# Optimization experiments

Hardware: AMD Instinct MI355X
Metric: run time of the kernel (lower is better)

The kernel has to match this reference:

```python
import jax, jax.numpy as jnp
import numpy as np

DIM = 256
WIN = 64
HEADS = 8
HEAD_DIM = DIM // HEADS
SCALE = HEAD_DIM ** -0.5


def setup_inputs() -> dict:
    key = jax.random.key(0)
    ks = jax.random.split(key, 8)
    B_ = 4096
    nW = 64
    x = jax.random.normal(ks[0], (B_, WIN, DIM), dtype=jnp.float32)
    mask = jax.random.normal(ks[1], (nW, WIN, WIN), dtype=jnp.float32)
    # qkv Linear(dim, 3*dim): stored as [dim, 3*dim] for x @ w
    w_qkv = jax.random.normal(ks[2], (DIM, 3 * DIM), dtype=jnp.float32) * (DIM ** -0.5)
    b_qkv = jax.random.normal(ks[3], (3 * DIM,), dtype=jnp.float32) * 0.02
    w_proj = jax.random.normal(ks[4], (DIM, DIM), dtype=jnp.float32) * (DIM ** -0.5)
    b_proj = jax.random.normal(ks[5], (DIM,), dtype=jnp.float32) * 0.02
    # relative_position_bias_table: [2*window_size - 1, num_heads], trunc_normal std=0.02
    bias_table = jax.random.normal(ks[6], (2 * WIN - 1, HEADS), dtype=jnp.float32) * 0.02
    return {"x": x, "mask": mask, "w_qkv": w_qkv, "b_qkv": b_qkv,
            "w_proj": w_proj, "b_proj": b_proj, "bias_table": bias_table}


def reference(x, mask, w_qkv, b_qkv, w_proj, b_proj, bias_table):
    B_, N, C = x.shape
    # qkv projection -> [3, B_, H, N, hd]
    qkv = (x @ w_qkv + b_qkv).reshape(B_, N, 3, HEADS, HEAD_DIM)
    qkv = jnp.transpose(qkv, (2, 0, 3, 1, 4))
    q, k, v = qkv[0], qkv[1], qkv[2]
    attn = jnp.einsum('bhnd,bhmd->bhnm', q * SCALE, k)  # [B_, H, N, N]
    # relative position bias gather: index [N, N] into table [2N-1, H]
    coords = jnp.arange(N)
    rel_idx = coords[:, None] - coords[None, :] + (N - 1)  # [N, N]
    rel_bias = bias_table[rel_idx]  # [N, N, H]
    attn = attn + jnp.transpose(rel_bias, (2, 0, 1))[None]  # broadcast over B_
    # mask add: [nW, N, N] broadcast over batch groups and heads
    nW = mask.shape[0]
    attn = attn.reshape(B_ // nW, nW, HEADS, N, N) + mask[None, :, None]
    attn = attn.reshape(B_, HEADS, N, N)
    attn = jax.nn.softmax(attn, axis=-1)  # dropout is identity in eval
    out = jnp.einsum('bhnm,bhmd->bhnd', attn, v)
    out = jnp.transpose(out, (0, 2, 1, 3)).reshape(B_, N, C)
    return out @ w_proj + b_proj
```

## Files before the change

kernel.cpp:

```cpp
#include <hip/hip_runtime.h>
#include <hip/hip_bf16.h>

#define DIM 256
#define WIN 64
#define HEADS 8
#define HD 32
#define NW 64

typedef __attribute__((ext_vector_type(8))) short bf16x8;
typedef __attribute__((ext_vector_type(4))) float f32x4;

#define XS 264
#define QS 40
#define VS 72
#define PS 72
#define HREG 7424
#define LDS_ELEMS (WIN * XS + HEADS * HREG)

__device__ __forceinline__ unsigned short f2bf(float f) {
  union { float f; unsigned u; } v; v.f = f;
  unsigned r = v.u + 0x7FFFu + ((v.u >> 16) & 1u);
  return (unsigned short)(r >> 16);
}

__device__ __forceinline__ bf16x8 ldf(const unsigned short* p) {
  return *reinterpret_cast<const bf16x8*>(p);
}

#define MFMA16(a, b, c) __builtin_amdgcn_mfma_f32_16x16x32_bf16(a, b, c, 0, 0, 0)

__global__ void prep_kernel(const float* __restrict__ w_qkv,
                            const float* __restrict__ b_qkv,
                            const float* __restrict__ w_proj,
                            const float* __restrict__ bias_table,
                            unsigned short* __restrict__ wqkv_t,
                            unsigned short* __restrict__ wproj_t,
                            float* __restrict__ bqkv_s,
                            float* __restrict__ rb) {
  const float SCALE = 0.1767766952966369f;
  int idx = blockIdx.x * blockDim.x + threadIdx.x;
  if (idx < 768 * 256) {
    int n = idx >> 8, k = idx & 255;
    float v = w_qkv[k * 768 + n];
    if (n < 256) v *= SCALE;
    wqkv_t[idx] = f2bf(v);
  }
  if (idx < 256 * 256) {
    int n = idx >> 8, k = idx & 255;
    wproj_t[idx] = f2bf(w_proj[k * 256 + n]);
  }
  if (idx < 768) {
    float v = b_qkv[idx];
    if (idx < 256) v *= SCALE;
    bqkv_s[idx] = v;
  }
  if (idx < HEADS * WIN * WIN) {
    int h = idx >> 12;
    int r = idx & 4095;
    int n = r >> 6, m = r & 63;
    rb[idx] = bias_table[(n - m + WIN - 1) * HEADS + h];
  }
}

__global__ __launch_bounds__(1024, 4) void fused_attn(
    const float* __restrict__ x,
    const float* __restrict__ mask,
    const float* __restrict__ b_proj,
    const unsigned short* __restrict__ wqkv_t,
    const unsigned short* __restrict__ wproj_t,
    const float* __restrict__ bqkv_s,
    const float* __restrict__ rb,
    float* __restrict__ out) {
  extern __shared__ unsigned short lds[];
  unsigned short* xs = lds;
  const int tid = threadIdx.x;
  const int wave = tid >> 6;
  const int lane = tid & 63;
  const int l16 = lane & 15;
  const int quad = lane >> 4;
  const int b = blockIdx.x;
  const int h = wave >> 1;
  const int sub = wave & 1;

  unsigned short* qh = lds + WIN * XS + h * HREG;
  unsigned short* kh = qh + 64 * QS;
  unsigned short* vth = qh + 2 * 64 * QS;
  unsigned short* ph = qh;

  const float4* xg = reinterpret_cast<const float4*>(x + (size_t)b * (WIN * DIM));
#pragma unroll
  for (int i = 0; i < 4; ++i) {
    int e = tid + i * 1024;
    float4 f = xg[e];
    int n = e >> 6;
    int c = (e & 63) << 2;
    ushort4 s4;
    s4.x = f2bf(f.x); s4.y = f2bf(f.y); s4.z = f2bf(f.z); s4.w = f2bf(f.w);
    *reinterpret_cast<ushort4*>(xs + n * XS + c) = s4;
  }
  __syncthreads();

  {
    f32x4 acc[3][4];
#pragma unroll
    for (int c = 0; c < 3; ++c)
#pragma unroll
      for (int rt = 0; rt < 4; ++rt) acc[c][rt] = (f32x4){0.f, 0.f, 0.f, 0.f};

#pragma unroll
    for (int kk = 0; kk < 8; ++kk) {
      int k0 = kk * 32 + quad * 8;
      bf16x8 a[4], bb[3];
#pragma unroll
      for (int rt = 0; rt < 4; ++rt) a[rt] = ldf(xs + (rt * 16 + l16) * XS + k0);
#pragma unroll
      for (int c = 0; c < 3; ++c) {
        int ctp = sub * 3 + c;
        int cbase = h * 32 + (ctp >> 1) * 256 + (ctp & 1) * 16;
        bb[c] = ldf(wqkv_t + (cbase + l16) * 256 + k0);
      }
#pragma unroll
      for (int c = 0; c < 3; ++c)
#pragma unroll
        for (int rt = 0; rt < 4; ++rt) acc[c][rt] = MFMA16(a[rt], bb[c], acc[c][rt]);
    }

#pragma unroll
    for (int c = 0; c < 3; ++c) {
      int ctp = sub * 3 + c;
      int cbase = h * 32 + (ctp >> 1) * 256 + (ctp & 1) * 16;
      float bias = bqkv_s[cbase + l16];
#pragma unroll
      for (int rt = 0; rt < 4; ++rt)
#pragma unroll
        for (int r = 0; r < 4; ++r) {
          int row = rt * 16 + quad * 4 + r;
          unsigned short bv = f2bf(acc[c][rt][r] + bias);
          if (ctp < 2)      qh[row * QS + ctp * 16 + l16] = bv;
          else if (ctp < 4) kh[row * QS + (ctp - 2) * 16 + l16] = bv;
          else              vth[((ctp - 4) * 16 + l16) * VS + row] = bv;
        }
    }
  }
  __syncthreads();

  {
    f32x4 sacc[2][4];
#pragma unroll
    for (int rt = 0; rt < 2; ++rt)
#pragma unroll
      for (int ct = 0; ct < 4; ++ct) sacc[rt][ct] = (f32x4){0.f, 0.f, 0.f, 0.f};

    bf16x8 a[2], bb[4];
#pragma unroll
    for (int rt = 0; rt < 2; ++rt)
      a[rt] = ldf(qh + (sub * 32 + rt * 16 + l16) * QS + quad * 8);
#pragma unroll
    for (int ct = 0; ct < 4; ++ct) bb[ct] = ldf(kh + (ct * 16 + l16) * QS + quad * 8);
#pragma unroll
    for (int rt = 0; rt < 2; ++rt)
#pragma unroll
      for (int ct = 0; ct < 4; ++ct) sacc[rt][ct] = MFMA16(a[rt], bb[ct], sacc[rt][ct]);

    const float* rbh = rb + h * (WIN * WIN);
    const float* mw = mask + (size_t)(b & (NW - 1)) * (WIN * WIN);
#pragma unroll
    for (int rt = 0; rt < 2; ++rt) {
#pragma unroll
      for (int r = 0; r < 4; ++r) {
        int row = sub * 32 + rt * 16 + quad * 4 + r;
        float vals[4];
#pragma unroll
        for (int ct = 0; ct < 4; ++ct) {
          int col = ct * 16 + l16;
          vals[ct] = sacc[rt][ct][r] + rbh[row * 64 + col] + mw[row * 64 + col];
        }
        float m = fmaxf(fmaxf(vals[0], vals[1]), fmaxf(vals[2], vals[3]));
#pragma unroll
        for (int o = 1; o < 16; o <<= 1) m = fmaxf(m, __shfl_xor(m, o, 64));
        float s = 0.f;
#pragma unroll
        for (int ct = 0; ct < 4; ++ct) { vals[ct] = __expf(vals[ct] - m); s += vals[ct]; }
#pragma unroll
        for (int o = 1; o < 16; o <<= 1) s += __shfl_xor(s, o, 64);
        float inv = 1.0f / s;
#pragma unroll
        for (int ct = 0; ct < 4; ++ct)
          ph[row * PS + ct * 16 + l16] = f2bf(vals[ct] * inv);
      }
    }
  }

  {
    f32x4 oacc[2][2];
#pragma unroll
    for (int jt = 0; jt < 2; ++jt)
#pragma unroll
      for (int rt = 0; rt < 2; ++rt) oacc[jt][rt] = (f32x4){0.f, 0.f, 0.f, 0.f};

#pragma unroll
    for (int km = 0; km < 2; ++km) {
      int k0 = km * 32 + quad * 8;
      bf16x8 a[2], bb[2];
#pragma unroll
      for (int rt = 0; rt < 2; ++rt)
        a[rt] = ldf(ph + (sub * 32 + rt * 16 + l16) * PS + k0);
#pragma unroll
      for (int jt = 0; jt < 2; ++jt) bb[jt] = ldf(vth + (jt * 16 + l16) * VS + k0);
#pragma unroll
      for (int jt = 0; jt < 2; ++jt)
#pragma unroll
        for (int rt = 0; rt < 2; ++rt) oacc[jt][rt] = MFMA16(a[rt], bb[jt], oacc[jt][rt]);
    }
#pragma unroll
    for (int jt = 0; jt < 2; ++jt)
#pragma unroll
      for (int rt = 0; rt < 2; ++rt)
#pragma unroll
        for (int r = 0; r < 4; ++r) {
          int row = sub * 32 + rt * 16 + quad * 4 + r;
          xs[row * XS + h * 32 + jt * 16 + l16] = f2bf(oacc[jt][rt][r]);
        }
  }
  __syncthreads();

  {
    f32x4 pacc[4];
#pragma unroll
    for (int rt = 0; rt < 4; ++rt) pacc[rt] = (f32x4){0.f, 0.f, 0.f, 0.f};
    const int col = h * 32 + sub * 16 + l16;

#pragma unroll
    for (int kk = 0; kk < 8; ++kk) {
      int k0 = kk * 32 + quad * 8;
      bf16x8 a[4], bb;
#pragma unroll
      for (int rt = 0; rt < 4; ++rt) a[rt] = ldf(xs + (rt * 16 + l16) * XS + k0);
      bb = ldf(wproj_t + col * 256 + k0);
#pragma unroll
      for (int rt = 0; rt < 4; ++rt) pacc[rt] = MFMA16(a[rt], bb, pacc[rt]);
    }
    float bias = b_proj[col];
#pragma unroll
    for (int rt = 0; rt < 4; ++rt)
#pragma unroll
      for (int r = 0; r < 4; ++r) {
        int row = rt * 16 + quad * 4 + r;
        out[(size_t)(b * WIN + row) * DIM + col] = pacc[rt][r] + bias;
      }
  }
}

extern "C" void kernel_launch(void* const* d_in, const int* in_sizes, int n_in,
                              void* d_out, int out_size, void* d_ws, size_t ws_size,
                              hipStream_t stream) {
  const float* x          = (const float*)d_in[0];
  const float* mask       = (const float*)d_in[1];
  const float* w_qkv      = (const float*)d_in[2];
  const float* b_qkv      = (const float*)d_in[3];
  const float* w_proj     = (const float*)d_in[4];
  const float* b_proj     = (const float*)d_in[5];
  const float* bias_table = (const float*)d_in[6];

  unsigned short* wqkv_t  = (unsigned short*)d_ws;
  unsigned short* wproj_t = wqkv_t + 768 * 256;
  float* bqkv_s           = (float*)(wproj_t + 256 * 256);
  float* rb               = bqkv_s + 768;

  prep_kernel<<<768, 256, 0, stream>>>(w_qkv, b_qkv, w_proj, bias_table,
                                       wqkv_t, wproj_t, bqkv_s, rb);

  (void)hipFuncSetAttribute((const void*)fused_attn,
                            hipFuncAttributeMaxDynamicSharedMemorySize,
                            LDS_ELEMS * 2);
  fused_attn<<<4096, 1024, LDS_ELEMS * 2, stream>>>(
      x, mask, b_proj, wqkv_t, wproj_t, bqkv_s, rb, (float*)d_out);
}
```

Measured before the change: 783.1 us.

## Process two heads per pass with 512-thread blocks and fused bias+mask table

```diff
diff --git a/kernel.cpp b/kernel.cpp
--- a/kernel.cpp
+++ b/kernel.cpp
@@ -14,8 +14,9 @@
 #define QS 40
 #define VS 72
 #define PS 72
-#define HREG 7424
-#define LDS_ELEMS (WIN * XS + HEADS * HREG)
+#define SS 72
+#define HREG (2 * 64 * QS + 32 * VS)
+#define LDS_ELEMS (WIN * XS + 2 * HREG + 64 * SS)
 
 __device__ __forceinline__ unsigned short f2bf(float f) {
   union { float f; unsigned u; } v; v.f = f;
@@ -33,10 +34,12 @@
                             const float* __restrict__ b_qkv,
                             const float* __restrict__ w_proj,
                             const float* __restrict__ bias_table,
+                            const float* __restrict__ mask,
                             unsigned short* __restrict__ wqkv_t,
                             unsigned short* __restrict__ wproj_t,
                             float* __restrict__ bqkv_s,
-                            float* __restrict__ rb) {
+                            float* __restrict__ rbp,
+                            int use_rbm) {
   const float SCALE = 0.1767766952966369f;
   int idx = blockIdx.x * blockDim.x + threadIdx.x;
   if (idx < 768 * 256) {
@@ -54,23 +57,34 @@
     if (idx < 256) v *= SCALE;
     bqkv_s[idx] = v;
   }
-  if (idx < HEADS * WIN * WIN) {
-    int h = idx >> 12;
-    int r = idx & 4095;
-    int n = r >> 6, m = r & 63;
-    rb[idx] = bias_table[(n - m + WIN - 1) * HEADS + h];
-  }
-}
-
-__global__ __launch_bounds__(1024, 4) void fused_attn(
+  if (use_rbm) {
+    if (idx < NW * HEADS * WIN * WIN) {
+      int w = idx >> 15;
+      int h = (idx >> 12) & 7;
+      int n = (idx >> 6) & 63;
+      int m = idx & 63;
+      rbp[idx] = bias_table[(n - m + WIN - 1) * HEADS + h] + mask[w * 4096 + n * 64 + m];
+    }
+  } else {
+    if (idx < HEADS * WIN * WIN) {
+      int h = idx >> 12;
+      int r = idx & 4095;
+      int n = r >> 6, m = r & 63;
+      rbp[idx] = bias_table[(n - m + WIN - 1) * HEADS + h];
+    }
+  }
+}
+
+__global__ __launch_bounds__(512, 4) void fused_attn(
     const float* __restrict__ x,
     const float* __restrict__ mask,
     const float* __restrict__ b_proj,
     const unsigned short* __restrict__ wqkv_t,
     const unsigned short* __restrict__ wproj_t,
     const float* __restrict__ bqkv_s,
-    const float* __restrict__ rb,
-    float* __restrict__ out) {
+    const float* __restrict__ rbp,
+    float* __restrict__ out,
+    int use_rbm) {
   extern __shared__ unsigned short lds[];
   unsigned short* xs = lds;
   const int tid = threadIdx.x;
@@ -79,18 +93,32 @@
   const int l16 = lane & 15;
   const int quad = lane >> 4;
   const int b = blockIdx.x;
-  const int h = wave >> 1;
-  const int sub = wave & 1;
-
-  unsigned short* qh = lds + WIN * XS + h * HREG;
+
+  const f32x4 zf = {0.f, 0.f, 0.f, 0.f};
+
+  const int h2 = wave >> 2;
+  const int rt = wave & 3;
+  const int rhalf = (wave >> 1) & 1;
+  const int cg = wave & 1;
+
+  unsigned short* hbase = lds + WIN * XS;
+  unsigned short* stage = hbase + 2 * HREG;
+
+  unsigned short* qh = hbase + h2 * HREG;
   unsigned short* kh = qh + 64 * QS;
   unsigned short* vth = qh + 2 * 64 * QS;
   unsigned short* ph = qh;
 
+  f32x4 pacc[2][4];
+#pragma unroll
+  for (int c2 = 0; c2 < 2; ++c2)
+#pragma unroll
+    for (int r2 = 0; r2 < 4; ++r2) pacc[c2][r2] = zf;
+
   const float4* xg = reinterpret_cast<const float4*>(x + (size_t)b * (WIN * DIM));
 #pragma unroll
-  for (int i = 0; i < 4; ++i) {
-    int e = tid + i * 1024;
+  for (int i = 0; i < 8; ++i) {
+    int e = tid + i * 512;
     float4 f = xg[e];
     int n = e >> 6;
     int c = (e & 63) << 2;
@@ -100,153 +128,152 @@
   }
   __syncthreads();
 
-  {
-    f32x4 acc[3][4];
-#pragma unroll
-    for (int c = 0; c < 3; ++c)
-#pragma unroll
-      for (int rt = 0; rt < 4; ++rt) acc[c][rt] = (f32x4){0.f, 0.f, 0.f, 0.f};
-
-#pragma unroll
-    for (int kk = 0; kk < 8; ++kk) {
-      int k0 = kk * 32 + quad * 8;
-      bf16x8 a[4], bb[3];
-#pragma unroll
-      for (int rt = 0; rt < 4; ++rt) a[rt] = ldf(xs + (rt * 16 + l16) * XS + k0);
+#pragma unroll 1
+  for (int p = 0; p < 4; ++p) {
+    {
+      unsigned short* qhw = hbase + h2 * HREG;
+      unsigned short* khw = qhw + 64 * QS;
+      unsigned short* vthw = qhw + 2 * 64 * QS;
+      const int hq = p * 2 + h2;
+      f32x4 qacc[3][2];
+#pragma unroll
+      for (int c = 0; c < 3; ++c)
+#pragma unroll
+        for (int rh = 0; rh < 2; ++rh) qacc[c][rh] = zf;
+
+#pragma unroll
+      for (int kk = 0; kk < 8; ++kk) {
+        int k0 = kk * 32 + quad * 8;
+        bf16x8 a0 = ldf(xs + (rhalf * 32 + l16) * XS + k0);
+        bf16x8 a1 = ldf(xs + (rhalf * 32 + 16 + l16) * XS + k0);
+#pragma unroll
+        for (int c = 0; c < 3; ++c) {
+          int ctp = cg * 3 + c;
+          int cbase = hq * 32 + (ctp >> 1) * 256 + (ctp & 1) * 16;
+          bf16x8 bb = ldf(wqkv_t + (cbase + l16) * 256 + k0);
+          qacc[c][0] = MFMA16(a0, bb, qacc[c][0]);
+          qacc[c][1] = MFMA16(a1, bb, qacc[c][1]);
+        }
+      }
 #pragma unroll
       for (int c = 0; c < 3; ++c) {
-        int ctp = sub * 3 + c;
-        int cbase = h * 32 + (ctp >> 1) * 256 + (ctp & 1) * 16;
-        bb[c] = ldf(wqkv_t + (cbase + l16) * 256 + k0);
-      }
-#pragma unroll
-      for (int c = 0; c < 3; ++c)
-#pragma unroll
-        for (int rt = 0; rt < 4; ++rt) acc[c][rt] = MFMA16(a[rt], bb[c], acc[c][rt]);
-    }
-
-#pragma unroll
-    for (int c = 0; c < 3; ++c) {
-      int ctp = sub * 3 + c;
-      int cbase = h * 32 + (ctp >> 1) * 256 + (ctp & 1) * 16;
-      float bias = bqkv_s[cbase + l16];
-#pragma unroll
-      for (int rt = 0; rt < 4; ++rt)
+        int ctp = cg * 3 + c;
+        int cbase = hq * 32 + (ctp >> 1) * 256 + (ctp & 1) * 16;
+        float bias = bqkv_s[cbase + l16];
+#pragma unroll
+        for (int rh = 0; rh < 2; ++rh)
+#pragma unroll
+          for (int r = 0; r < 4; ++r) {
+            int row = rhalf * 32 + rh * 16 + quad * 4 + r;
+            unsigned short bv = f2bf(qacc[c][rh][r] + bias);
+            if (ctp < 2)      qhw[row * QS + ctp * 16 + l16] = bv;
+            else if (ctp < 4) khw[row * QS + (ctp - 2) * 16 + l16] = bv;
+            else              vthw[((ctp - 4) * 16 + l16) * VS + row] = bv;
+          }
+      }
+    }
+    __syncthreads();
+
+    const int h = p * 2 + h2;
+    f32x4 sacc[4];
+    {
+      bf16x8 a = ldf(qh + (rt * 16 + l16) * QS + quad * 8);
+#pragma unroll
+      for (int ct = 0; ct < 4; ++ct) {
+        bf16x8 bb = ldf(kh + (ct * 16 + l16) * QS + quad * 8);
+        sacc[ct] = MFMA16(a, bb, zf);
+      }
+    }
+    __syncthreads();
+
+    {
+      const float* rbw;
+      const float* mw = nullptr;
+      if (use_rbm) {
+        rbw = rbp + ((size_t)((b & (NW - 1)) * HEADS + h)) * 4096;
+      } else {
+        rbw = rbp + h * 4096;
+        mw = mask + (size_t)(b & (NW - 1)) * 4096;
+      }
+#pragma unroll
+      for (int r = 0; r < 4; ++r) {
+        int row = rt * 16 + quad * 4 + r;
+        float vals[4];
+#pragma unroll
+        for (int ct = 0; ct < 4; ++ct) {
+          int col = ct * 16 + l16;
+          float add = use_rbm ? rbw[row * 64 + col]
+                              : (rbw[row * 64 + col] + mw[row * 64 + col]);
+          vals[ct] = sacc[ct][r] + add;
+        }
+        float m = fmaxf(fmaxf(vals[0], vals[1]), fmaxf(vals[2], vals[3]));
+#pragma unroll
+        for (int o = 1; o < 16; o <<= 1) m = fmaxf(m, __shfl_xor(m, o, 64));
+        float s = 0.f;
+#pragma unroll
+        for (int ct = 0; ct < 4; ++ct) { vals[ct] = __expf(vals[ct] - m); s += vals[ct]; }
+#pragma unroll
+        for (int o = 1; o < 16; o <<= 1) s += __shfl_xor(s, o, 64);
+        float inv = 1.0f / s;
+#pragma unroll
+        for (int ct = 0; ct < 4; ++ct)
+          ph[row * PS + ct * 16 + l16] = f2bf(vals[ct] * inv);
+      }
+    }
+
+    {
+      f32x4 oacc[2] = {zf, zf};
+#pragma unroll
+      for (int km = 0; km < 2; ++km) {
+        int k0 = km * 32 + quad * 8;
+        bf16x8 a = ldf(ph + (rt * 16 + l16) * PS + k0);
+#pragma unroll
+        for (int jt = 0; jt < 2; ++jt) {
+          bf16x8 bb = ldf(vth + (jt * 16 + l16) * VS + k0);
+          oacc[jt] = MFMA16(a, bb, oacc[jt]);
+        }
+      }
+#pragma unroll
+      for (int jt = 0; jt < 2; ++jt)
 #pragma unroll
         for (int r = 0; r < 4; ++r) {
           int row = rt * 16 + quad * 4 + r;
-          unsigned short bv = f2bf(acc[c][rt][r] + bias);
-          if (ctp < 2)      qh[row * QS + ctp * 16 + l16] = bv;
-          else if (ctp < 4) kh[row * QS + (ctp - 2) * 16 + l16] = bv;
-          else              vth[((ctp - 4) * 16 + l16) * VS + row] = bv;
-        }
-    }
-  }
-  __syncthreads();
-
-  {
-    f32x4 sacc[2][4];
-#pragma unroll
-    for (int rt = 0; rt < 2; ++rt)
-#pragma unroll
-      for (int ct = 0; ct < 4; ++ct) sacc[rt][ct] = (f32x4){0.f, 0.f, 0.f, 0.f};
-
-    bf16x8 a[2], bb[4];
-#pragma unroll
-    for (int rt = 0; rt < 2; ++rt)
-      a[rt] = ldf(qh + (sub * 32 + rt * 16 + l16) * QS + quad * 8);
-#pragma unroll
-    for (int ct = 0; ct < 4; ++ct) bb[ct] = ldf(kh + (ct * 16 + l16) * QS + quad * 8);
-#pragma unroll
-    for (int rt = 0; rt < 2; ++rt)
-#pragma unroll
-      for (int ct = 0; ct < 4; ++ct) sacc[rt][ct] = MFMA16(a[rt], bb[ct], sacc[rt][ct]);
-
-    const float* rbh = rb + h * (WIN * WIN);
-    const float* mw = mask + (size_t)(b & (NW - 1)) * (WIN * WIN);
-#pragma unroll
-    for (int rt = 0; rt < 2; ++rt) {
+          stage[row * SS + h2 * 32 + jt * 16 + l16] = f2bf(oacc[jt][r]);
+        }
+    }
+    __syncthreads();
+
+    {
+#pragma unroll
+      for (int hb = 0; hb < 2; ++hb) {
+        int hh = p * 2 + hb;
+        bf16x8 bb[2];
+#pragma unroll
+        for (int c2 = 0; c2 < 2; ++c2) {
+          int ct = wave * 2 + c2;
+          bb[c2] = ldf(wproj_t + (ct * 16 + l16) * 256 + hh * 32 + quad * 8);
+        }
+#pragma unroll
+        for (int r2 = 0; r2 < 4; ++r2) {
+          bf16x8 a = ldf(stage + (r2 * 16 + l16) * SS + hb * 32 + quad * 8);
+#pragma unroll
+          for (int c2 = 0; c2 < 2; ++c2)
+            pacc[c2][r2] = MFMA16(a, bb[c2], pacc[c2][r2]);
+        }
+      }
+    }
+  }
+
+#pragma unroll
+  for (int c2 = 0; c2 < 2; ++c2) {
+    int col = wave * 32 + c2 * 16 + l16;
+    float bias = b_proj[col];
+#pragma unroll
+    for (int r2 = 0; r2 < 4; ++r2)
 #pragma unroll
       for (int r = 0; r < 4; ++r) {
-        int row = sub * 32 + rt * 16 + quad * 4 + r;
-        float vals[4];
-#pragma unroll
-        for (int ct = 0; ct < 4; ++ct) {
-          int col = ct * 16 + l16;
-          vals[ct] = sacc[rt][ct][r] + rbh[row * 64 + col] + mw[row * 64 + col];
-        }
-        float m = fmaxf(fmaxf(vals[0], vals[1]), fmaxf(vals[2], vals[3]));
-#pragma unroll
-        for (int o = 1; o < 16; o <<= 1) m = fmaxf(m, __shfl_xor(m, o, 64));
-        float s = 0.f;
-#pragma unroll
-        for (int ct = 0; ct < 4; ++ct) { vals[ct] = __expf(vals[ct] - m); s += vals[ct]; }
-#pragma unroll
-        for (int o = 1; o < 16; o <<= 1) s += __shfl_xor(s, o, 64);
-        float inv = 1.0f / s;
-#pragma unroll
-        for (int ct = 0; ct < 4; ++ct)
-          ph[row * PS + ct * 16 + l16] = f2bf(vals[ct] * inv);
-      }
-    }
-  }
-
-  {
-    f32x4 oacc[2][2];
-#pragma unroll
-    for (int jt = 0; jt < 2; ++jt)
-#pragma unroll
-      for (int rt = 0; rt < 2; ++rt) oacc[jt][rt] = (f32x4){0.f, 0.f, 0.f, 0.f};
-
-#pragma unroll
-    for (int km = 0; km < 2; ++km) {
-      int k0 = km * 32 + quad * 8;
-      bf16x8 a[2], bb[2];
-#pragma unroll
-      for (int rt = 0; rt < 2; ++rt)
-        a[rt] = ldf(ph + (sub * 32 + rt * 16 + l16) * PS + k0);
-#pragma unroll
-      for (int jt = 0; jt < 2; ++jt) bb[jt] = ldf(vth + (jt * 16 + l16) * VS + k0);
-#pragma unroll
-      for (int jt = 0; jt < 2; ++jt)
-#pragma unroll
-        for (int rt = 0; rt < 2; ++rt) oacc[jt][rt] = MFMA16(a[rt], bb[jt], oacc[jt][rt]);
-    }
-#pragma unroll
-    for (int jt = 0; jt < 2; ++jt)
-#pragma unroll
-      for (int rt = 0; rt < 2; ++rt)
-#pragma unroll
-        for (int r = 0; r < 4; ++r) {
-          int row = sub * 32 + rt * 16 + quad * 4 + r;
-          xs[row * XS + h * 32 + jt * 16 + l16] = f2bf(oacc[jt][rt][r]);
-        }
-  }
-  __syncthreads();
-
-  {
-    f32x4 pacc[4];
-#pragma unroll
-    for (int rt = 0; rt < 4; ++rt) pacc[rt] = (f32x4){0.f, 0.f, 0.f, 0.f};
-    const int col = h * 32 + sub * 16 + l16;
-
-#pragma unroll
-    for (int kk = 0; kk < 8; ++kk) {
-      int k0 = kk * 32 + quad * 8;
-      bf16x8 a[4], bb;
-#pragma unroll
-      for (int rt = 0; rt < 4; ++rt) a[rt] = ldf(xs + (rt * 16 + l16) * XS + k0);
-      bb = ldf(wproj_t + col * 256 + k0);
-#pragma unroll
-      for (int rt = 0; rt < 4; ++rt) pacc[rt] = MFMA16(a[rt], bb, pacc[rt]);
-    }
-    float bias = b_proj[col];
-#pragma unroll
-    for (int rt = 0; rt < 4; ++rt)
-#pragma unroll
-      for (int r = 0; r < 4; ++r) {
-        int row = rt * 16 + quad * 4 + r;
-        out[(size_t)(b * WIN + row) * DIM + col] = pacc[rt][r] + bias;
+        int row = r2 * 16 + quad * 4 + r;
+        out[(size_t)(b * WIN + row) * DIM + col] = pacc[c2][r2][r] + bias;
       }
   }
 }
@@ -265,14 +292,18 @@
   unsigned short* wqkv_t  = (unsigned short*)d_ws;
   unsigned short* wproj_t = wqkv_t + 768 * 256;
   float* bqkv_s           = (float*)(wproj_t + 256 * 256);
-  float* rb               = bqkv_s + 768;
-
-  prep_kernel<<<768, 256, 0, stream>>>(w_qkv, b_qkv, w_proj, bias_table,
-                                       wqkv_t, wproj_t, bqkv_s, rb);
+  float* rbp              = bqkv_s + 768;
+
+  const size_t need_rbm = 527360 + (size_t)NW * HEADS * WIN * WIN * 4;
+  int use_rbm = (ws_size >= need_rbm) ? 1 : 0;
+  int pgrid = use_rbm ? 8192 : 768;
+
+  prep_kernel<<<pgrid, 256, 0, stream>>>(w_qkv, b_qkv, w_proj, bias_table, mask,
+                                         wqkv_t, wproj_t, bqkv_s, rbp, use_rbm);
 
   (void)hipFuncSetAttribute((const void*)fused_attn,
                             hipFuncAttributeMaxDynamicSharedMemorySize,
                             LDS_ELEMS * 2);
-  fused_attn<<<4096, 1024, LDS_ELEMS * 2, stream>>>(
-      x, mask, b_proj, wqkv_t, wproj_t, bqkv_s, rb, (float*)d_out);
-}
+  fused_attn<<<4096, 512, LDS_ELEMS * 2, stream>>>(
+      x, mask, b_proj, wqkv_t, wproj_t, bqkv_s, rbp, (float*)d_out, use_rbm);
+}
```

Measured after the change: 1.145 ms. 1.46x slower.
